# Kernel tuning notes

Hardware: AMD Instinct MI355X
Metric: run time of the kernel (lower is better)

The kernel has to match this reference:

```python
import jax, jax.numpy as jnp
import numpy as np

N_ATOMS = 200000
N_BONDS = 400000
MAX_NB = 6
HID = 128
ATOM_FDIM = 151
BOND_FDIM = 165
N_HEADS = 2


def _layer_norm(x, g, b, eps=1e-5):
    mu = jnp.mean(x, axis=-1, keepdims=True)
    var = jnp.var(x, axis=-1, keepdims=True)
    return g * (x - mu) * jax.lax.rsqrt(var + eps) + b


def setup_inputs() -> dict:
    key = jax.random.key(0)
    ks = jax.random.split(key, 12)
    s = 0.05  # weight init scale
    return {
        'f_atoms': jax.random.normal(ks[0], (N_ATOMS, ATOM_FDIM), jnp.float32),
        'f_bonds': jax.random.normal(ks[1], (N_BONDS, BOND_FDIM), jnp.float32),
        'a2a': jax.random.randint(ks[2], (N_ATOMS, MAX_NB), 0, N_ATOMS, jnp.int32),
        'a2b': jax.random.randint(ks[3], (N_ATOMS, MAX_NB), 0, N_BONDS, jnp.int32),
        'W_i': jax.random.normal(ks[4], (ATOM_FDIM, HID), jnp.float32) * s,
        'b_i': jnp.zeros((HID,), jnp.float32),
        'ln1_g': jnp.ones((HID,), jnp.float32),
        'ln1_b': jnp.zeros((HID,), jnp.float32),
        'Wh_q': jax.random.normal(ks[5], (N_HEADS, HID + BOND_FDIM, HID), jnp.float32) * s,
        'bh_q': jnp.zeros((N_HEADS, HID), jnp.float32),
        'Wh_k': jax.random.normal(ks[6], (N_HEADS, HID + BOND_FDIM, HID), jnp.float32) * s,
        'bh_k': jnp.zeros((N_HEADS, HID), jnp.float32),
        'Wh_v': jax.random.normal(ks[7], (N_HEADS, HID + BOND_FDIM, HID), jnp.float32) * s,
        'bh_v': jnp.zeros((N_HEADS, HID), jnp.float32),
        'W_o': jax.random.normal(ks[8], (N_HEADS * HID, HID), jnp.float32) * s,
        'b_o': jnp.zeros((HID,), jnp.float32),
        'ln2_g': jnp.ones((HID,), jnp.float32),
        'ln2_b': jnp.zeros((HID,), jnp.float32),
    }


def reference(f_atoms, f_bonds, a2a, a2b, W_i, b_i, ln1_g, ln1_b,
              Wh_q, bh_q, Wh_k, bh_k, Wh_v, bh_v, W_o, b_o, ln2_g, ln2_b):
    # Input projection of raw atom features: dropout(layernorm(act(W_i x)))
    # (dropout = identity in eval).
    h0 = _layer_norm(jax.nn.relu(f_atoms @ W_i + b_i), ln1_g, ln1_b)  # [N, H]

    # Graph gather: neighbor atom hidden states + incident bond raw features.
    nei_a = h0[a2a]       # [N, nb, H]   irregular gather
    nei_b = f_bonds[a2b]  # [N, nb, Fb]  irregular gather
    # Aggregate messages once; shared across Q/K/V branches and heads.
    msg = jnp.concatenate([nei_a, nei_b], axis=-1).sum(axis=1)  # [N, H+Fb]

    def branch(Wh, bh):  # Wh: [heads, H+Fb, H] -> [N, heads, H]
        return jax.nn.relu(h0[:, None, :] + jnp.einsum('nf,efh->neh', msg, Wh) + bh)

    Q = branch(Wh_q, bh_q)  # [N, heads, H]
    K = branch(Wh_k, bh_k)
    V = branch(Wh_v, bh_v)

    # Attention across the heads axis (per atom).
    scores = jnp.einsum('nqh,nkh->nqk', Q, K) / jnp.sqrt(jnp.float32(HID))
    attn = jax.nn.softmax(scores, axis=-1)
    x = jnp.einsum('nqk,nkh->nqh', attn, V).reshape(Q.shape[0], -1)  # [N, heads*H]

    x_out = x @ W_o + b_o  # [N, H]
    # Residual sublayer connection.
    f_atoms_out = h0 + _layer_norm(x_out, ln2_g, ln2_b)
    return f_atoms_out
```

## Files before the change

### kernel.cpp

```cpp
#include <hip/hip_runtime.h>

typedef unsigned short u16;
typedef unsigned int u32;
typedef __attribute__((ext_vector_type(8))) short s8v;
typedef __attribute__((ext_vector_type(4))) float f4v;
typedef __attribute__((ext_vector_type(2))) float f2v;

#define NATOMS 200000
#define NBONDS 400000

__device__ __forceinline__ float b2f(u32 u) {
    union { u32 i; float f; } v; v.i = u << 16; return v.f;
}
__device__ __forceinline__ u16 f2b(float f) {
    union { float f; u32 i; } v; v.f = f;
    u32 r = v.i + 0x7fffu + ((v.i >> 16) & 1u);
    return (u16)(r >> 16);
}
__device__ __forceinline__ uint4 pack8(const float* f) {
    uint4 o;
    o.x = (u32)f2b(f[0]) | ((u32)f2b(f[1]) << 16);
    o.y = (u32)f2b(f[2]) | ((u32)f2b(f[3]) << 16);
    o.z = (u32)f2b(f[4]) | ((u32)f2b(f[5]) << 16);
    o.w = (u32)f2b(f[6]) | ((u32)f2b(f[7]) << 16);
    return o;
}
__device__ __forceinline__ void acc8(uint4 u, float* a) {
    a[0] += b2f(u.x & 0xffffu); a[1] += b2f(u.x >> 16);
    a[2] += b2f(u.y & 0xffffu); a[3] += b2f(u.y >> 16);
    a[4] += b2f(u.z & 0xffffu); a[5] += b2f(u.z >> 16);
    a[6] += b2f(u.w & 0xffffu); a[7] += b2f(u.w >> 16);
}

__global__ void k_wprep(const float* __restrict__ Whq, const float* __restrict__ Whk,
                        const float* __restrict__ Whv, const float* __restrict__ Wo,
                        const float* __restrict__ Wi,
                        u16* __restrict__ wallw, u16* __restrict__ wow, u16* __restrict__ wiw) {
    int t = blockIdx.x * 256 + threadIdx.x;
    if (t < 245760) {
        int ks = t / 24576, rem = t % 24576;
        int n = rem >> 5, kk = rem & 31;
        int k = ks * 32 + kk;
        int hg = n / 48, r48 = n % 48;
        int branch = r48 >> 4, r16i = r48 & 15;
        int head = r16i >> 3, h = hg * 8 + (r16i & 7);
        const float* Wp = (branch == 0) ? Whq : ((branch == 1) ? Whk : Whv);
        float val = (k < 293) ? Wp[(head * 293 + k) * 128 + h] : 0.f;
        wallw[t] = f2b(val);
    } else if (t < 278528) {
        int u = t - 245760;
        int ks = u >> 12, n = (u >> 5) & 127, kk = u & 31;
        int k = ks * 32 + kk;
        wow[u] = f2b(Wo[k * 128 + n]);
    } else if (t < 299008) {
        int u = t - 278528;
        int ks = u >> 12, n = (u >> 5) & 127, kk = u & 31;
        int k = ks * 32 + kk;
        wiw[u] = (k < 151) ? f2b(Wi[k * 128 + n]) : (u16)0;
    }
}

__global__ void k_bond16(const float* __restrict__ fb, u16* __restrict__ fbw) {
    int t = blockIdx.x * 256 + threadIdx.x;
    if (t >= NBONDS * 21) return;
    u32 b = (u32)t / 21u, c = (u32)t % 21u;
    const float* src = fb + (size_t)b * 165 + c * 8;
    float a[8];
    #pragma unroll
    for (int q = 0; q < 8; q++) a[q] = ((int)(c * 8 + q) < 165) ? src[q] : 0.f;
    *(uint4*)&fbw[(size_t)b * 168 + c * 8] = pack8(a);
}

#define H0_SMEM (64 * 168 * 2 + 64 * 132 * 4)
__global__ __launch_bounds__(256) void k_h0(
    const float* __restrict__ fa, const u16* __restrict__ wiw,
    const float* __restrict__ bi, const float* __restrict__ g1, const float* __restrict__ b1,
    u16* __restrict__ h0w) {
    extern __shared__ char smem[];
    u16* la = (u16*)smem;
    float* lo = (float*)(smem + 21504);
    const int tid = threadIdx.x;
    const size_t abase = (size_t)blockIdx.x * 64;

    for (int i = tid; i < 64 * 151; i += 256) {
        int r = i / 151, c = i - r * 151;
        la[r * 168 + c] = f2b(fa[(abase + r) * 151 + c]);
    }
    for (int i = tid; i < 64 * 17; i += 256) {
        int r = i / 17, c = i - r * 17;
        la[r * 168 + 151 + c] = 0;
    }
    __syncthreads();

    const int w = tid >> 6, l = tid & 63;
    const int r16 = l & 15, kq = l >> 4;
    f4v acc[4][2];
    #pragma unroll
    for (int m = 0; m < 4; m++)
        #pragma unroll
        for (int c = 0; c < 2; c++)
            #pragma unroll
            for (int v = 0; v < 4; v++) acc[m][c][v] = 0.f;

    #pragma unroll
    for (int ks = 0; ks < 5; ++ks) {
        s8v af[4];
        #pragma unroll
        for (int m = 0; m < 4; m++)
            af[m] = *(const s8v*)&la[(m * 16 + r16) * 168 + ks * 32 + kq * 8];
        #pragma unroll
        for (int c = 0; c < 2; c++) {
            int n = w * 32 + c * 16 + r16;
            s8v bf = *(const s8v*)&wiw[ks * 4096 + n * 32 + kq * 8];
            #pragma unroll
            for (int m = 0; m < 4; m++)
                acc[m][c] = __builtin_amdgcn_mfma_f32_16x16x32_bf16(af[m], bf, acc[m][c], 0, 0, 0);
        }
    }
    #pragma unroll
    for (int c = 0; c < 2; c++) {
        int col = w * 32 + c * 16 + r16;
        float bias = bi[col];
        #pragma unroll
        for (int m = 0; m < 4; m++) {
            #pragma unroll
            for (int v = 0; v < 4; v++) {
                int row = m * 16 + kq * 4 + v;
                lo[row * 132 + col] = fmaxf(acc[m][c][v] + bias, 0.f);
            }
        }
    }
    __syncthreads();

    const int ga = tid >> 2, sb = tid & 3;
    float vals[32], s = 0.f, s2 = 0.f;
    #pragma unroll
    for (int j = 0; j < 32; j++) {
        float v = lo[ga * 132 + sb + 4 * j];
        vals[j] = v; s += v; s2 += v * v;
    }
    s += __shfl_xor(s, 1); s += __shfl_xor(s, 2);
    s2 += __shfl_xor(s2, 1); s2 += __shfl_xor(s2, 2);
    float mu = s * (1.f / 128.f), var = s2 * (1.f / 128.f) - mu * mu;
    float rs = rsqrtf(var + 1e-5f);
    u16* orow = h0w + (abase + ga) * 128;
    #pragma unroll
    for (int j = 0; j < 32; j++) {
        int col = sb + 4 * j;
        orow[col] = f2b(g1[col] * (vals[j] - mu) * rs + b1[col]);
    }
}

#define SMEM_FUSED 53248
__global__ __launch_bounds__(1024) void k_fused(
    const u16* __restrict__ h0w, const u16* __restrict__ fbw,
    const int* __restrict__ a2a, const int* __restrict__ a2b,
    const u16* __restrict__ wallw, const u16* __restrict__ wow,
    const float* __restrict__ bhq, const float* __restrict__ bhk, const float* __restrict__ bhv,
    const float* __restrict__ bo, const float* __restrict__ g2, const float* __restrict__ b2,
    float* __restrict__ out) {
    extern __shared__ char smem[];
    float* sco2 = (float*)smem;
    u16* lx = (u16*)(smem + 16384);
    float* attn = (float*)(smem + 50176);
    float* pp = (float*)(smem + 51200);

    const int tid = threadIdx.x;
    const size_t abase = (size_t)blockIdx.x * 64;
    const int w = tid >> 6, l = tid & 63;
    const int r16 = l & 15, kq = l >> 4;
    const u32 xmask = (u32)((r16 & 7) << 4);

    const u16* bp = wallw + (size_t)(w * 48 + r16) * 32 + kq * 8;
    s8v bfA0 = *(const s8v*)&bp[0];
    s8v bfA1 = *(const s8v*)&bp[512];
    s8v bfA2 = *(const s8v*)&bp[1024];

    #pragma unroll
    for (int ii = 0; ii < 3; ++ii) {
        int i = tid + ii * 1024;
        if (i < 2560) {
            int r = i / 40, c = i - r * 40;
            uint4 val;
            if (c < 37) {
                float a[8] = {0, 0, 0, 0, 0, 0, 0, 0};
                if (c < 16) {
                    const int* na = a2a + (abase + r) * 6;
                    #pragma unroll
                    for (int j = 0; j < 6; j++)
                        acc8(*(const uint4*)&h0w[(size_t)(u32)na[j] * 128 + c * 8], a);
                } else {
                    const int* nb = a2b + (abase + r) * 6;
                    #pragma unroll
                    for (int j = 0; j < 6; j++)
                        acc8(*(const uint4*)&fbw[(size_t)(u32)nb[j] * 168 + (c - 16) * 8], a);
                }
                val = pack8(a);
            } else {
                val = (uint4){0, 0, 0, 0};
            }
            *(uint4*)(smem + (((u32)(r * 640 + c * 16)) ^ ((u32)((r & 7) << 4)))) = val;
        }
    }
    __syncthreads();

    f4v acc[4][3];
    #pragma unroll
    for (int m = 0; m < 4; m++)
        #pragma unroll
        for (int c = 0; c < 3; c++)
            #pragma unroll
            for (int v = 0; v < 4; v++) acc[m][c][v] = 0.f;

    s8v bfB0, bfB1, bfB2;
    #pragma unroll
    for (int kp = 0; kp < 5; ++kp) {
        {
            const int ks = 2 * kp;
            const u16* nb = bp + (size_t)(ks + 1) * 24576;
            bfB0 = *(const s8v*)&nb[0];
            bfB1 = *(const s8v*)&nb[512];
            bfB2 = *(const s8v*)&nb[1024];
            #pragma unroll
            for (int m = 0; m < 4; m++) {
                s8v af = *(const s8v*)(smem +
                    (((u32)((m * 16 + r16) * 640 + ks * 64 + kq * 16)) ^ xmask));
                acc[m][0] = __builtin_amdgcn_mfma_f32_16x16x32_bf16(af, bfA0, acc[m][0], 0, 0, 0);
                acc[m][1] = __builtin_amdgcn_mfma_f32_16x16x32_bf16(af, bfA1, acc[m][1], 0, 0, 0);
                acc[m][2] = __builtin_amdgcn_mfma_f32_16x16x32_bf16(af, bfA2, acc[m][2], 0, 0, 0);
            }
        }
        {
            const int ks = 2 * kp + 1;
            if (kp < 4) {
                const u16* nb = bp + (size_t)(ks + 1) * 24576;
                bfA0 = *(const s8v*)&nb[0];
                bfA1 = *(const s8v*)&nb[512];
                bfA2 = *(const s8v*)&nb[1024];
            }
            #pragma unroll
            for (int m = 0; m < 4; m++) {
                s8v af = *(const s8v*)(smem +
                    (((u32)((m * 16 + r16) * 640 + ks * 64 + kq * 16)) ^ xmask));
                acc[m][0] = __builtin_amdgcn_mfma_f32_16x16x32_bf16(af, bfB0, acc[m][0], 0, 0, 0);
                acc[m][1] = __builtin_amdgcn_mfma_f32_16x16x32_bf16(af, bfB1, acc[m][1], 0, 0, 0);
                acc[m][2] = __builtin_amdgcn_mfma_f32_16x16x32_bf16(af, bfB2, acc[m][2], 0, 0, 0);
            }
        }
    }

    const int head = r16 >> 3;
    const int h = w * 8 + (r16 & 7);
    float h0r[4][4];
    #pragma unroll
    for (int m = 0; m < 4; m++)
        #pragma unroll
        for (int v = 0; v < 4; v++)
            h0r[m][v] = b2f(h0w[(abase + m * 16 + kq * 4 + v) * 128 + h]);
    const float bq = bhq[head * 128 + h];
    const float bk = bhk[head * 128 + h];
    const float bv = bhv[head * 128 + h];

    __syncthreads();

    #pragma unroll
    for (int m = 0; m < 4; m++) {
        #pragma unroll
        for (int v = 0; v < 4; v++) {
            int row = m * 16 + kq * 4 + v;
            float q  = fmaxf(acc[m][0][v] + h0r[m][v] + bq, 0.f);
            float kk = fmaxf(acc[m][1][v] + h0r[m][v] + bk, 0.f);
            float vv = fmaxf(acc[m][2][v] + h0r[m][v] + bv, 0.f);
            acc[m][2][v] = vv;
            float kx = __shfl_xor(kk, 8);
            float pA = q * kk;
            float pB = q * kx;
            pA += __shfl_xor(pA, 1); pA += __shfl_xor(pA, 2); pA += __shfl_xor(pA, 4);
            pB += __shfl_xor(pB, 1); pB += __shfl_xor(pB, 2); pB += __shfl_xor(pB, 4);
            if ((r16 & 7) == ((m * 4 + v) & 7)) {
                f2v pr; pr[0] = pA; pr[1] = pB;
                *(f2v*)&sco2[(w * 64 + row) * 4 + head * 2] = pr;
            }
        }
    }
    __syncthreads();

    if (tid < 128) {
        int atom = tid >> 1, qh = tid & 1;
        float ss = 0.f, sx = 0.f;
        #pragma unroll
        for (int ww = 0; ww < 16; ww++) {
            f2v p = *(const f2v*)&sco2[(ww * 64 + atom) * 4 + qh * 2];
            ss += p[0]; sx += p[1];
        }
        const float sc = 0.08838834764831845f;
        ss *= sc; sx *= sc;
        float mm = fmaxf(ss, sx);
        float e0 = __expf(ss - mm), e1 = __expf(sx - mm);
        float inv = 1.f / (e0 + e1);
        attn[atom * 4 + qh * 2] = e0 * inv;
        attn[atom * 4 + qh * 2 + 1] = e1 * inv;
    }
    __syncthreads();

    #pragma unroll
    for (int m = 0; m < 4; m++) {
        #pragma unroll
        for (int v = 0; v < 4; v++) {
            int row = m * 16 + kq * 4 + v;
            f2v a = *(const f2v*)&attn[row * 4 + head * 2];
            float vv = acc[m][2][v];
            float vx = __shfl_xor(vv, 8);
            lx[row * 264 + head * 128 + h] = f2b(a[0] * vv + a[1] * vx);
        }
    }
    __syncthreads();

    const int mb = w >> 2, ch = w & 3;
    f4v oa0, oa1;
    #pragma unroll
    for (int v = 0; v < 4; v++) { oa0[v] = 0.f; oa1[v] = 0.f; }
    const u16* xp = lx + (mb * 16 + r16) * 264 + kq * 8;
    const u16* wp2 = wow + (ch * 32 + r16) * 32 + kq * 8;
    #pragma unroll
    for (int ks = 0; ks < 8; ks++) {
        s8v a = *(const s8v*)&xp[ks * 32];
        s8v b0 = *(const s8v*)&wp2[ks * 4096];
        s8v b1 = *(const s8v*)&wp2[ks * 4096 + 512];
        oa0 = __builtin_amdgcn_mfma_f32_16x16x32_bf16(a, b0, oa0, 0, 0, 0);
        oa1 = __builtin_amdgcn_mfma_f32_16x16x32_bf16(a, b1, oa1, 0, 0, 0);
    }

    const int col0 = ch * 32 + r16, col1 = col0 + 16;
    const float bo0 = bo[col0], bo1 = bo[col1];
    float xo0[4], xo1[4], sv[4], s2v[4];
    #pragma unroll
    for (int v = 0; v < 4; v++) {
        xo0[v] = oa0[v] + bo0;
        xo1[v] = oa1[v] + bo1;
        float s = xo0[v] + xo1[v];
        float s2 = xo0[v] * xo0[v] + xo1[v] * xo1[v];
        s += __shfl_xor(s, 1); s += __shfl_xor(s, 2);
        s += __shfl_xor(s, 4); s += __shfl_xor(s, 8);
        s2 += __shfl_xor(s2, 1); s2 += __shfl_xor(s2, 2);
        s2 += __shfl_xor(s2, 4); s2 += __shfl_xor(s2, 8);
        sv[v] = s; s2v[v] = s2;
    }
    if (r16 == 0) {
        #pragma unroll
        for (int v = 0; v < 4; v++) {
            int row = mb * 16 + kq * 4 + v;
            pp[row * 8 + ch * 2] = sv[v];
            pp[row * 8 + ch * 2 + 1] = s2v[v];
        }
    }
    __syncthreads();

    const float ga0 = g2[col0], ga1 = g2[col1];
    const float bb0 = b2[col0], bb1 = b2[col1];
    #pragma unroll
    for (int v = 0; v < 4; v++) {
        int row = mb * 16 + kq * 4 + v;
        f4v p0 = *(f4v*)&pp[row * 8];
        f4v p1 = *(f4v*)&pp[row * 8 + 4];
        float ssum = p0[0] + p0[2] + p1[0] + p1[2];
        float s2sum = p0[1] + p0[3] + p1[1] + p1[3];
        float mu = ssum * (1.f / 128.f);
        float var = s2sum * (1.f / 128.f) - mu * mu;
        float rs = rsqrtf(var + 1e-5f);
        float* orow = out + (abase + row) * 128;
        orow[col0] = ga0 * (xo0[v] - mu) * rs + bb0 + b2f(h0w[(abase + row) * 128 + col0]);
        orow[col1] = ga1 * (xo1[v] - mu) * rs + bb1 + b2f(h0w[(abase + row) * 128 + col1]);
    }
}

extern "C" void kernel_launch(void* const* d_in, const int* in_sizes, int n_in,
                              void* d_out, int out_size, void* d_ws, size_t ws_size,
                              hipStream_t stream) {
    const float* f_atoms = (const float*)d_in[0];
    const float* f_bonds = (const float*)d_in[1];
    const int* a2a = (const int*)d_in[2];
    const int* a2b = (const int*)d_in[3];
    const float* W_i = (const float*)d_in[4];
    const float* b_i = (const float*)d_in[5];
    const float* ln1g = (const float*)d_in[6];
    const float* ln1b = (const float*)d_in[7];
    const float* Whq = (const float*)d_in[8];
    const float* bhq = (const float*)d_in[9];
    const float* Whk = (const float*)d_in[10];
    const float* bhk = (const float*)d_in[11];
    const float* Whv = (const float*)d_in[12];
    const float* bhv = (const float*)d_in[13];
    const float* Wo = (const float*)d_in[14];
    const float* bo = (const float*)d_in[15];
    const float* ln2g = (const float*)d_in[16];
    const float* ln2b = (const float*)d_in[17];
    float* out = (float*)d_out;

    char* ws = (char*)d_ws;
    u16* h0w = (u16*)(ws + 0);
    u16* fbw = (u16*)(ws + 51200000);
    u16* wallw = (u16*)(ws + 185600000);
    u16* wow = (u16*)(ws + 186091520);
    u16* wiw = (u16*)(ws + 186157056);

    hipFuncSetAttribute(reinterpret_cast<const void*>(k_fused),
                        hipFuncAttributeMaxDynamicSharedMemorySize, SMEM_FUSED);

    k_wprep<<<1168, 256, 0, stream>>>(Whq, Whk, Whv, Wo, W_i, wallw, wow, wiw);
    k_bond16<<<32813, 256, 0, stream>>>(f_bonds, fbw);
    k_h0<<<3125, 256, H0_SMEM, stream>>>(f_atoms, wiw, b_i, ln1g, ln1b, h0w);
    k_fused<<<3125, 1024, SMEM_FUSED, stream>>>(h0w, fbw, a2a, a2b, wallw, wow,
                                                bhq, bhk, bhv, bo, ln2g, ln2b, out);
}
```

Before: 575.7 us.

## Precompute bond-message sums in separate kernel and stage h0 tile in LDS

Moves the per-atom gather-and-sum of bond features out of the fused kernel into a new k_msgb kernel that writes a bf16 message buffer. The fused kernel then reads that buffer contiguously instead of doing scattered bond gathers. It also stages the block's own h0 rows in shared memory for reuse in the epilogue. The cost is an extra kernel launch, an extra global write and read of about 67 MB, and more LDS per block (76.8 KB), which may reduce occupancy of the 1024-thread fused kernel.

After: 599.5 us. 1.04x slower.

```diff
diff --git a/kernel.cpp b/kernel.cpp
--- a/kernel.cpp
+++ b/kernel.cpp
@@ -71,6 +71,19 @@
     *(uint4*)&fbw[(size_t)b * 168 + c * 8] = pack8(a);
 }
 
+__global__ void k_msgb(const u16* __restrict__ fbw, const int* __restrict__ a2b,
+                       u16* __restrict__ msgb) {
+    int t = blockIdx.x * 256 + threadIdx.x;
+    if (t >= NATOMS * 21) return;
+    u32 atom = (u32)t / 21u, c = (u32)t % 21u;
+    const int* nb = a2b + (size_t)atom * 6;
+    float a[8] = {0, 0, 0, 0, 0, 0, 0, 0};
+    #pragma unroll
+    for (int j = 0; j < 6; j++)
+        acc8(*(const uint4*)&fbw[(size_t)(u32)nb[j] * 168 + c * 8], a);
+    *(uint4*)&msgb[(size_t)atom * 168 + c * 8] = pack8(a);
+}
+
 #define H0_SMEM (64 * 168 * 2 + 64 * 132 * 4)
 __global__ __launch_bounds__(256) void k_h0(
     const float* __restrict__ fa, const u16* __restrict__ wiw,
@@ -151,19 +164,20 @@
     }
 }
 
-#define SMEM_FUSED 53248
+#define SMEM_FUSED 76800
 __global__ __launch_bounds__(1024) void k_fused(
-    const u16* __restrict__ h0w, const u16* __restrict__ fbw,
-    const int* __restrict__ a2a, const int* __restrict__ a2b,
+    const u16* __restrict__ h0w, const u16* __restrict__ msgb,
+    const int* __restrict__ a2a,
     const u16* __restrict__ wallw, const u16* __restrict__ wow,
     const float* __restrict__ bhq, const float* __restrict__ bhk, const float* __restrict__ bhv,
     const float* __restrict__ bo, const float* __restrict__ g2, const float* __restrict__ b2,
     float* __restrict__ out) {
     extern __shared__ char smem[];
-    float* sco2 = (float*)smem;
-    u16* lx = (u16*)(smem + 16384);
-    float* attn = (float*)(smem + 50176);
-    float* pp = (float*)(smem + 51200);
+    u16* lx = (u16*)smem;
+    u16* lh0 = (u16*)(smem + 40960);
+    float* sco2 = (float*)(smem + 57344);
+    float* attn = (float*)(smem + 73728);
+    float* pp = (float*)(smem + 74752);
 
     const int tid = threadIdx.x;
     const size_t abase = (size_t)blockIdx.x * 64;
@@ -176,26 +190,26 @@
     s8v bfA1 = *(const s8v*)&bp[512];
     s8v bfA2 = *(const s8v*)&bp[1024];
 
+    {
+        int r = tid >> 4, cc = (tid & 15) << 3;
+        *(uint4*)&lh0[r * 128 + cc] = *(const uint4*)&h0w[(abase + r) * 128 + cc];
+    }
+
     #pragma unroll
     for (int ii = 0; ii < 3; ++ii) {
         int i = tid + ii * 1024;
         if (i < 2560) {
             int r = i / 40, c = i - r * 40;
             uint4 val;
-            if (c < 37) {
+            if (c < 16) {
+                const int* na = a2a + (abase + r) * 6;
                 float a[8] = {0, 0, 0, 0, 0, 0, 0, 0};
-                if (c < 16) {
-                    const int* na = a2a + (abase + r) * 6;
-                    #pragma unroll
-                    for (int j = 0; j < 6; j++)
-                        acc8(*(const uint4*)&h0w[(size_t)(u32)na[j] * 128 + c * 8], a);
-                } else {
-                    const int* nb = a2b + (abase + r) * 6;
-                    #pragma unroll
-                    for (int j = 0; j < 6; j++)
-                        acc8(*(const uint4*)&fbw[(size_t)(u32)nb[j] * 168 + (c - 16) * 8], a);
-                }
+                #pragma unroll
+                for (int j = 0; j < 6; j++)
+                    acc8(*(const uint4*)&h0w[(size_t)(u32)na[j] * 128 + c * 8], a);
                 val = pack8(a);
+            } else if (c < 37) {
+                val = *(const uint4*)&msgb[(abase + r) * 168 + (c - 16) * 8];
             } else {
                 val = (uint4){0, 0, 0, 0};
             }
@@ -251,26 +265,18 @@
 
     const int head = r16 >> 3;
     const int h = w * 8 + (r16 & 7);
-    float h0r[4][4];
-    #pragma unroll
-    for (int m = 0; m < 4; m++)
-        #pragma unroll
-        for (int v = 0; v < 4; v++)
-            h0r[m][v] = b2f(h0w[(abase + m * 16 + kq * 4 + v) * 128 + h]);
     const float bq = bhq[head * 128 + h];
     const float bk = bhk[head * 128 + h];
     const float bv = bhv[head * 128 + h];
-
-    __syncthreads();
-
     #pragma unroll
     for (int m = 0; m < 4; m++) {
         #pragma unroll
         for (int v = 0; v < 4; v++) {
             int row = m * 16 + kq * 4 + v;
-            float q  = fmaxf(acc[m][0][v] + h0r[m][v] + bq, 0.f);
-            float kk = fmaxf(acc[m][1][v] + h0r[m][v] + bk, 0.f);
-            float vv = fmaxf(acc[m][2][v] + h0r[m][v] + bv, 0.f);
+            float h0v = b2f(lh0[row * 128 + h]);
+            float q  = fmaxf(acc[m][0][v] + h0v + bq, 0.f);
+            float kk = fmaxf(acc[m][1][v] + h0v + bk, 0.f);
+            float vv = fmaxf(acc[m][2][v] + h0v + bv, 0.f);
             acc[m][2][v] = vv;
             float kx = __shfl_xor(kk, 8);
             float pA = q * kk;
@@ -369,8 +375,8 @@
         float var = s2sum * (1.f / 128.f) - mu * mu;
         float rs = rsqrtf(var + 1e-5f);
         float* orow = out + (abase + row) * 128;
-        orow[col0] = ga0 * (xo0[v] - mu) * rs + bb0 + b2f(h0w[(abase + row) * 128 + col0]);
-        orow[col1] = ga1 * (xo1[v] - mu) * rs + bb1 + b2f(h0w[(abase + row) * 128 + col1]);
+        orow[col0] = ga0 * (xo0[v] - mu) * rs + bb0 + b2f(lh0[row * 128 + col0]);
+        orow[col1] = ga1 * (xo1[v] - mu) * rs + bb1 + b2f(lh0[row * 128 + col1]);
     }
 }
 
@@ -400,9 +406,10 @@
     char* ws = (char*)d_ws;
     u16* h0w = (u16*)(ws + 0);
     u16* fbw = (u16*)(ws + 51200000);
-    u16* wallw = (u16*)(ws + 185600000);
-    u16* wow = (u16*)(ws + 186091520);
-    u16* wiw = (u16*)(ws + 186157056);
+    u16* msgb = (u16*)(ws + 185600000);
+    u16* wallw = (u16*)(ws + 252800000);
+    u16* wow = (u16*)(ws + 253291520);
+    u16* wiw = (u16*)(ws + 253357056);
 
     hipFuncSetAttribute(reinterpret_cast<const void*>(k_fused),
                         hipFuncAttributeMaxDynamicSharedMemorySize, SMEM_FUSED);
@@ -410,6 +417,7 @@
     k_wprep<<<1168, 256, 0, stream>>>(Whq, Whk, Whv, Wo, W_i, wallw, wow, wiw);
     k_bond16<<<32813, 256, 0, stream>>>(f_bonds, fbw);
     k_h0<<<3125, 256, H0_SMEM, stream>>>(f_atoms, wiw, b_i, ln1g, ln1b, h0w);
-    k_fused<<<3125, 1024, SMEM_FUSED, stream>>>(h0w, fbw, a2a, a2b, wallw, wow,
+    k_msgb<<<16407, 256, 0, stream>>>(fbw, a2b, msgb);
+    k_fused<<<3125, 1024, SMEM_FUSED, stream>>>(h0w, msgb, a2a, wallw, wow,
                                                 bhq, bhk, bhv, bo, ln2g, ln2b, out);
 }
```
